# Performance work log

Measured on AMD Instinct MI355X. Metric: run time of the kernel, lower is better.

## Reference

```python
import jax, jax.numpy as jnp
import numpy as np

L, D, H, DFF, V, N, B, C = 4, 512, 8, 2048, 32000, 512, 16, 3
DH = D // H
EPS = 1e-6


def _sinusoid_pe(n, d):
    pos = np.arange(n)[:, None].astype(np.float32)
    div = np.exp(np.arange(0, d, 2).astype(np.float32) * (-np.log(10000.0) / d))
    pe = np.zeros((n, d), np.float32)
    pe[:, 0::2] = np.sin(pos * div)
    pe[:, 1::2] = np.cos(pos * div)
    return jnp.asarray(pe)


def _ln(x, g, b):
    m = x.mean(-1, keepdims=True)
    v = ((x - m) ** 2).mean(-1, keepdims=True)
    return (x - m) * jax.lax.rsqrt(v + EPS) * g + b


def setup_inputs() -> dict:
    key = jax.random.key(0)
    ks = jax.random.split(key, 12)
    rn = lambda k, s: jax.random.normal(k, s, jnp.float32) * 0.02
    return {
        "src": jax.random.randint(ks[0], (N, B, 1), 0, V, jnp.int32),
        "lengths": jnp.full((B,), N, jnp.int32),
        "emb_table": rn(ks[1], (V, D)),
        "ln1_g": jnp.ones((L, D)), "ln1_b": jnp.zeros((L, D)),
        "Wq": rn(ks[2], (L, D, D)), "bq": jnp.zeros((L, D)),
        "Wk": rn(ks[3], (L, D, D)), "bk": jnp.zeros((L, D)),
        "Wv": rn(ks[4], (L, D, D)), "bv": jnp.zeros((L, D)),
        "Wo": rn(ks[5], (L, D, D)), "bo": jnp.zeros((L, D)),
        "ln2_g": jnp.ones((L, D)), "ln2_b": jnp.zeros((L, D)),
        "W1": rn(ks[6], (L, D, DFF)), "b1": jnp.zeros((L, DFF)),
        "W2": rn(ks[7], (L, DFF, D)), "b2": jnp.zeros((L, D)),
        "lnf_g": jnp.ones((D,)), "lnf_b": jnp.zeros((D,)),
        "inf_W": rn(ks[8], (2 * D, C)),
    }


def reference(src, lengths, emb_table, ln1_g, ln1_b, Wq, bq, Wk, bk, Wv, bv,
              Wo, bo, ln2_g, ln2_b, W1, b1, W2, b2, lnf_g, lnf_b, inf_W):
    # embeddings: lookup * sqrt(d) + sinusoidal PE (onmt Embeddings)
    emb = emb_table[src[:, :, 0]] * jnp.sqrt(jnp.float32(D))  # [N,B,D]
    x = (emb + _sinusoid_pe(N, D)[:, None, :]).transpose(1, 0, 2)  # [B,N,D]
    key_pad = jnp.arange(N)[None, :] >= lengths[:, None]  # [B,N] True = pad
    for l in range(L):
        h = _ln(x, ln1_g[l], ln1_b[l])
        q = (h @ Wq[l] + bq[l]).reshape(B, N, H, DH).transpose(0, 2, 1, 3)
        k = (h @ Wk[l] + bk[l]).reshape(B, N, H, DH).transpose(0, 2, 1, 3)
        v = (h @ Wv[l] + bv[l]).reshape(B, N, H, DH).transpose(0, 2, 1, 3)
        scores = jnp.einsum('bhqd,bhkd->bhqk', q, k) / jnp.sqrt(jnp.float32(DH))
        scores = jnp.where(key_pad[:, None, None, :], -1e9, scores)
        attn = jax.nn.softmax(scores, -1)
        ctx = jnp.einsum('bhqk,bhkd->bhqd', attn, v).transpose(0, 2, 1, 3).reshape(B, N, D)
        x = x + ctx @ Wo[l] + bo[l]
        h2 = _ln(x, ln2_g[l], ln2_b[l])
        x = x + jax.nn.relu(h2 @ W1[l] + b1[l]) @ W2[l] + b2[l]
    x = _ln(x, lnf_g, lnf_b)  # [B,N,D]
    attn_res = x.transpose(1, 0, 2)  # [N,B,D]
    # pairwise scorer: Linear(concat(x_i, x_j)) == x_i @ W[:D] + x_j @ W[D:]
    la = x @ inf_W[:D]   # [B,N,C]
    lb = x @ inf_W[D:]   # [B,N,C]
    logits = la[:, :, None, :] + lb[:, None, :, :]  # [B,N,N,C]
    inf_result = jax.nn.log_softmax(logits, -1).reshape(B, N * N, C)
    inf_result = jnp.swapaxes(inf_result, 0, 1)  # [N*N,B,C]
    return (attn_res, inf_result)
```

## Files before the change

kernel.cpp:

```cpp
#include <hip/hip_runtime.h>

constexpr int L = 4, D = 512, H = 8, DFF = 2048, NSEQ = 512, B = 16, C = 3;
constexpr int DH = D / H;
constexpr int M = B * NSEQ;
constexpr int BND = B * NSEQ * D;

typedef short bf16x8 __attribute__((ext_vector_type(8)));
typedef float f32x4 __attribute__((ext_vector_type(4)));

__device__ __forceinline__ float blo(unsigned u) { return __uint_as_float(u << 16); }
__device__ __forceinline__ float bhi(unsigned u) { return __uint_as_float(u & 0xffff0000u); }
__device__ __forceinline__ unsigned short f2b(float f) {
    unsigned u = __float_as_uint(f);
    u += 0x7fffu + ((u >> 16) & 1u);
    return (unsigned short)(u >> 16);
}
__device__ __forceinline__ void gload_lds16(const void* g, void* l) {
    __builtin_amdgcn_global_load_lds(
        (const __attribute__((address_space(1))) void*)g,
        (__attribute__((address_space(3))) void*)l, 16, 0, 0);
}

__device__ __forceinline__ float block_sum256(float v, float* r4) {
#pragma unroll
    for (int o = 32; o > 0; o >>= 1) v += __shfl_xor(v, o, 64);
    if ((threadIdx.x & 63) == 0) r4[threadIdx.x >> 6] = v;
    __syncthreads();
    return r4[0] + r4[1] + r4[2] + r4[3];
}

__global__ __launch_bounds__(256) void conv_t_kernel(
    const float* __restrict__ in, unsigned short* __restrict__ out, int K, int N)
{
    __shared__ float t[32][33];
    int n0 = blockIdx.x * 32, k0 = blockIdx.y * 32;
    const float* ip = in + (size_t)blockIdx.z * K * N;
    unsigned short* op = out + (size_t)blockIdx.z * K * N;
    int tx = threadIdx.x & 31, ty = threadIdx.x >> 5;
#pragma unroll
    for (int i = 0; i < 4; i++)
        t[ty + i * 8][tx] = ip[(size_t)(k0 + ty + i * 8) * N + n0 + tx];
    __syncthreads();
#pragma unroll
    for (int i = 0; i < 4; i++)
        op[(size_t)(n0 + ty + i * 8) * K + k0 + tx] = f2b(t[tx][ty + i * 8]);
}

__global__ __launch_bounds__(256) void embed_pe_kernel(
    const int* __restrict__ src, const float* __restrict__ emb,
    float* __restrict__ x)
{
    int idx = blockIdx.x * 256 + threadIdx.x;
    int d = idx & (D - 1);
    int t = idx >> 9;
    int n = t & (NSEQ - 1);
    int b = t >> 9;
    int tok = src[n * B + b];
    float e = emb[(size_t)tok * D + d] * 22.627416997969522f;
    float div = expf((float)(d & ~1) * -0.01798894603797866f);
    float ang = (float)n * div;
    float pe = (d & 1) ? cosf(ang) : sinf(ang);
    x[idx] = e + pe;
}

template<int BF16OUT>
__global__ __launch_bounds__(256) void ln_kernel(
    const float* __restrict__ in, const float* __restrict__ g,
    const float* __restrict__ bt, void* __restrict__ outv)
{
    __shared__ float ra[4], rb[4];
    int row = blockIdx.x, tid = threadIdx.x;
    const float* p = in + (size_t)row * D;
    float v0 = p[tid], v1 = p[tid + 256];
    float mean = block_sum256(v0 + v1, ra) * (1.0f / D);
    float d0 = v0 - mean, d1 = v1 - mean;
    float var = block_sum256(d0 * d0 + d1 * d1, rb) * (1.0f / D);
    float rstd = rsqrtf(var + 1e-6f);
    float o0 = d0 * rstd * g[tid] + bt[tid];
    float o1 = d1 * rstd * g[tid + 256] + bt[tid + 256];
    if (BF16OUT) {
        unsigned short* o = (unsigned short*)outv + (size_t)row * D;
        o[tid] = f2b(o0); o[tid + 256] = f2b(o1);
    } else {
        float* o = (float*)outv + (size_t)row * D;
        o[tid] = o0; o[tid + 256] = o1;
    }
}

template<int ADD, int RELU, int BF16OUT, int VTRANS>
__global__ __launch_bounds__(256) void mfma_gemm(
    const unsigned short* __restrict__ A,
    const unsigned short* __restrict__ Wt,
    const float* __restrict__ bias,
    void* __restrict__ outv, int Kdim, int Ndim)
{
    __shared__ __align__(16) unsigned short As[128 * 32];
    __shared__ __align__(16) unsigned short Bs[128 * 32];
    int tid = threadIdx.x;
    int wave = tid >> 6, lane = tid & 63;
    int lr = lane & 15, lc = lane >> 4;
    int m0 = blockIdx.y * 128, n0 = blockIdx.x * 128;
    int wm = (wave >> 1) * 64, wn = (wave & 1) * 64;
    int srow = tid >> 2;
    int scol = (tid & 3) << 3;

    const unsigned short* Ab = A + ((size_t)m0 + srow) * Kdim + scol;
    const unsigned short* Bb = Wt + ((size_t)n0 + srow) * Kdim + scol;
    unsigned short* AsW = As + wave * 512;
    unsigned short* BsW = Bs + wave * 512;

    f32x4 acc[4][4] = {};

    for (int kb = 0; kb < Kdim; kb += 32) {
        gload_lds16(Ab + kb, AsW);
        gload_lds16(Ab + kb + (size_t)64 * Kdim, AsW + 2048);
        gload_lds16(Bb + kb, BsW);
        gload_lds16(Bb + kb + (size_t)64 * Kdim, BsW + 2048);
        __syncthreads();

        bf16x8 aF[4], bF[4];
#pragma unroll
        for (int i = 0; i < 4; i++) {
            aF[i] = *reinterpret_cast<const bf16x8*>(&As[(wm + i * 16 + lr) * 32 + lc * 8]);
            bF[i] = *reinterpret_cast<const bf16x8*>(&Bs[(wn + i * 16 + lr) * 32 + lc * 8]);
        }
#pragma unroll
        for (int i = 0; i < 4; i++)
#pragma unroll
            for (int j = 0; j < 4; j++)
                acc[i][j] = __builtin_amdgcn_mfma_f32_16x16x32_bf16(aF[i], bF[j], acc[i][j], 0, 0, 0);
        __syncthreads();
    }

#pragma unroll
    for (int i = 0; i < 4; i++) {
        int grow = m0 + wm + i * 16 + lc * 4;
#pragma unroll
        for (int j = 0; j < 4; j++) {
            int gcol = n0 + wn + j * 16 + lr;
            float bv = bias[gcol];
#pragma unroll
            for (int r = 0; r < 4; r++) {
                float v = acc[i][j][r] + bv;
                if (RELU) v = fmaxf(v, 0.0f);
                if (VTRANS) {
                    int rowg = grow + r;
                    size_t off = ((size_t)((rowg >> 9) << 9) + gcol) * NSEQ + (rowg & (NSEQ - 1));
                    ((unsigned short*)outv)[off] = f2b(v);
                } else {
                    size_t off = (size_t)(grow + r) * Ndim + gcol;
                    if (BF16OUT)      ((unsigned short*)outv)[off] = f2b(v);
                    else if (ADD)     ((float*)outv)[off] += v;
                    else              ((float*)outv)[off] = v;
                }
            }
        }
    }
}

__global__ __launch_bounds__(256, 3) void attn_mfma_kernel(
    const unsigned short* __restrict__ qg, const unsigned short* __restrict__ kg,
    const unsigned short* __restrict__ vtg, const int* __restrict__ lengths,
    unsigned short* __restrict__ ctx)
{
    __shared__ __align__(16) unsigned short Ks[64 * 64];
    __shared__ __align__(16) unsigned short Vt[64 * 64];
    __shared__ __align__(16) unsigned short Ps[64 * 64];

    int tid = threadIdx.x;
    int wave = tid >> 6, lane = tid & 63;
    int lr = lane & 15, lc = lane >> 4;
    int qt = blockIdx.x, hh = blockIdx.y, b = blockIdx.z;
    int len = lengths[b];

    const unsigned short* qbase  = qg  + ((size_t)(b * NSEQ + qt * 64)) * D + hh * DH;
    const unsigned short* kbase  = kg  + ((size_t)(b * NSEQ)) * D + hh * DH;
    const unsigned short* vtbase = vtg + ((size_t)(b * D + hh * DH)) * NSEQ;

    auto SW = [](int row, int colbyte) { return row * 128 + (colbyte ^ ((row & 7) << 4)); };

#pragma unroll
    for (int it = 0; it < 2; it++) {
        int c = it * 256 + tid;
        int row = c >> 3, d0 = (c & 7) << 3;
        uint4 t = *reinterpret_cast<const uint4*>(qbase + (size_t)row * D + d0);
        *reinterpret_cast<uint4*>((char*)Ps + SW(row, d0 * 2)) = t;
    }
    __syncthreads();
    bf16x8 aQ[2];
#pragma unroll
    for (int s = 0; s < 2; s++)
        aQ[s] = *reinterpret_cast<const bf16x8*>((char*)Ps + SW(wave * 16 + lr, s * 64 + lc * 16));

    f32x4 o[4] = {};
    float mrow[4], lrow[4];
#pragma unroll
    for (int r = 0; r < 4; r++) { mrow[r] = -INFINITY; lrow[r] = 0.0f; }

    for (int kt = 0; kt < 8; kt++) {
#pragma unroll
        for (int it = 0; it < 2; it++) {
            int c = it * 256 + tid;
            int row = c >> 3, d0 = (c & 7) << 3;
            uint4 t = *reinterpret_cast<const uint4*>(kbase + (size_t)(kt * 64 + row) * D + d0);
            *reinterpret_cast<uint4*>((char*)Ks + SW(row, d0 * 2)) = t;
            uint4 tv = *reinterpret_cast<const uint4*>(vtbase + (size_t)row * NSEQ + kt * 64 + d0);
            *reinterpret_cast<uint4*>((char*)Vt + SW(row, d0 * 2)) = tv;
        }
        __syncthreads();

        f32x4 sacc[4] = {};
#pragma unroll
        for (int kf = 0; kf < 4; kf++) {
#pragma unroll
            for (int s = 0; s < 2; s++) {
                bf16x8 bK = *reinterpret_cast<const bf16x8*>((char*)Ks + SW(kf * 16 + lr, s * 64 + lc * 16));
                sacc[kf] = __builtin_amdgcn_mfma_f32_16x16x32_bf16(aQ[s], bK, sacc[kf], 0, 0, 0);
            }
        }

        float p[4][4], tm[4];
#pragma unroll
        for (int r = 0; r < 4; r++) tm[r] = -INFINITY;
#pragma unroll
        for (int kf = 0; kf < 4; kf++) {
            int col = kt * 64 + kf * 16 + lr;
            bool ok = col < len;
#pragma unroll
            for (int r = 0; r < 4; r++) {
                float sv = ok ? sacc[kf][r] * 0.125f : -1e9f;
                p[kf][r] = sv;
                tm[r] = fmaxf(tm[r], sv);
            }
        }
#pragma unroll
        for (int r = 0; r < 4; r++) {
#pragma unroll
            for (int msk = 1; msk < 16; msk <<= 1)
                tm[r] = fmaxf(tm[r], __shfl_xor(tm[r], msk, 64));
        }
        float alpha[4], ps[4];
#pragma unroll
        for (int r = 0; r < 4; r++) {
            float nm = fmaxf(mrow[r], tm[r]);
            alpha[r] = __expf(mrow[r] - nm);
            mrow[r] = nm;
            ps[r] = 0.0f;
        }
#pragma unroll
        for (int kf = 0; kf < 4; kf++)
#pragma unroll
            for (int r = 0; r < 4; r++) {
                float e = __expf(p[kf][r] - mrow[r]);
                p[kf][r] = e;
                ps[r] += e;
            }
#pragma unroll
        for (int r = 0; r < 4; r++) {
#pragma unroll
            for (int msk = 1; msk < 16; msk <<= 1)
                ps[r] += __shfl_xor(ps[r], msk, 64);
            lrow[r] = lrow[r] * alpha[r] + ps[r];
        }

#pragma unroll
        for (int kf = 0; kf < 4; kf++)
#pragma unroll
            for (int r = 0; r < 4; r++)
                *reinterpret_cast<unsigned short*>(
                    (char*)Ps + SW(wave * 16 + lc * 4 + r, (kf * 16 + lr) * 2)) = f2b(p[kf][r]);

#pragma unroll
        for (int df = 0; df < 4; df++)
#pragma unroll
            for (int r = 0; r < 4; r++)
                o[df][r] *= alpha[r];

#pragma unroll
        for (int s = 0; s < 2; s++) {
            bf16x8 pa = *reinterpret_cast<const bf16x8*>((char*)Ps + SW(wave * 16 + lr, s * 64 + lc * 16));
#pragma unroll
            for (int df = 0; df < 4; df++) {
                bf16x8 vb = *reinterpret_cast<const bf16x8*>((char*)Vt + SW(df * 16 + lr, s * 64 + lc * 16));
                o[df] = __builtin_amdgcn_mfma_f32_16x16x32_bf16(pa, vb, o[df], 0, 0, 0);
            }
        }
        __syncthreads();
    }

    unsigned short* obase = ctx + ((size_t)(b * NSEQ + qt * 64 + wave * 16)) * D + hh * DH;
#pragma unroll
    for (int r = 0; r < 4; r++) {
        float inv = 1.0f / lrow[r];
        int q = lc * 4 + r;
#pragma unroll
        for (int df = 0; df < 4; df++)
            obase[(size_t)q * D + df * 16 + lr] = f2b(o[df][r] * inv);
    }
}

__global__ __launch_bounds__(256) void store_attnres(
    const float* __restrict__ hf, float* __restrict__ out)
{
    int idx = blockIdx.x * 256 + threadIdx.x;
    int d  = idx & (D - 1);
    int nb = idx >> 9;
    int b  = nb & (B - 1);
    int n  = nb >> 4;
    out[idx] = hf[((size_t)(b * NSEQ + n)) * D + d];
}

__global__ __launch_bounds__(256) void lalb_kernel(
    const float* __restrict__ hf, const float* __restrict__ infW,
    float* __restrict__ la, float* __restrict__ lb)
{
    __shared__ float r24[24];
    int t = blockIdx.x, tid = threadIdx.x;
    const float* p = hf + (size_t)t * D;
    float x0 = p[tid], x1 = p[tid + 256];
    float s[6];
#pragma unroll
    for (int c = 0; c < 3; c++) {
        s[c]     = x0 * infW[(size_t)tid * C + c]         + x1 * infW[(size_t)(tid + 256) * C + c];
        s[3 + c] = x0 * infW[(size_t)(tid + 512) * C + c] + x1 * infW[(size_t)(tid + 768) * C + c];
    }
#pragma unroll
    for (int c = 0; c < 6; c++)
#pragma unroll
        for (int o = 32; o > 0; o >>= 1) s[c] += __shfl_xor(s[c], o, 64);
    if ((tid & 63) == 0) {
#pragma unroll
        for (int c = 0; c < 6; c++) r24[c * 4 + (tid >> 6)] = s[c];
    }
    __syncthreads();
    if (tid < 6) {
        float v = r24[tid * 4] + r24[tid * 4 + 1] + r24[tid * 4 + 2] + r24[tid * 4 + 3];
        if (tid < 3) la[(size_t)t * C + tid] = v;
        else         lb[(size_t)t * C + tid - 3] = v;
    }
}

__global__ __launch_bounds__(256) void logits_kernel(
    const float* __restrict__ la, const float* __restrict__ lb,
    float* __restrict__ out)
{
    int idx = blockIdx.x * 256 + threadIdx.x;
    int b  = idx & (B - 1);
    int ij = idx >> 4;
    int j  = ij & (NSEQ - 1);
    int i  = ij >> 9;
    const float* pa = la + ((size_t)(b * NSEQ + i)) * C;
    const float* pb = lb + ((size_t)(b * NSEQ + j)) * C;
    float l0 = pa[0] + pb[0];
    float l1 = pa[1] + pb[1];
    float l2 = pa[2] + pb[2];
    float m = fmaxf(l0, fmaxf(l1, l2));
    float lse = m + logf(__expf(l0 - m) + __expf(l1 - m) + __expf(l2 - m));
    out[(size_t)idx * 3 + 0] = l0 - lse;
    out[(size_t)idx * 3 + 1] = l1 - lse;
    out[(size_t)idx * 3 + 2] = l2 - lse;
}

extern "C" void kernel_launch(void* const* d_in, const int* in_sizes, int n_in,
                              void* d_out, int out_size, void* d_ws, size_t ws_size,
                              hipStream_t stream)
{
    const int*   src     = (const int*)  d_in[0];
    const int*   lengths = (const int*)  d_in[1];
    const float* emb     = (const float*)d_in[2];
    const float* ln1_g   = (const float*)d_in[3];
    const float* ln1_b   = (const float*)d_in[4];
    const float* Wq      = (const float*)d_in[5];
    const float* bq      = (const float*)d_in[6];
    const float* Wk      = (const float*)d_in[7];
    const float* bk      = (const float*)d_in[8];
    const float* Wv      = (const float*)d_in[9];
    const float* bv      = (const float*)d_in[10];
    const float* Wo      = (const float*)d_in[11];
    const float* bo      = (const float*)d_in[12];
    const float* ln2_g   = (const float*)d_in[13];
    const float* ln2_b   = (const float*)d_in[14];
    const float* W1      = (const float*)d_in[15];
    const float* b1      = (const float*)d_in[16];
    const float* W2      = (const float*)d_in[17];
    const float* b2      = (const float*)d_in[18];
    const float* lnf_g   = (const float*)d_in[19];
    const float* lnf_b   = (const float*)d_in[20];
    const float* infW    = (const float*)d_in[21];

    char* wsb = (char*)d_ws;
    float*          x   = (float*)wsb;
    unsigned short* h   = (unsigned short*)(wsb + (size_t)BND * 4);
    unsigned short* wts = (unsigned short*)(wsb + (size_t)BND * 4 + (size_t)BND * 2);
    char*           big = wsb + (size_t)BND * 4 + (size_t)BND * 2 + 25165824;

    unsigned short* qbm = (unsigned short*)big;
    unsigned short* kbm = qbm + (size_t)M * D;
    unsigned short* vtm = kbm + (size_t)M * D;
    unsigned short* ffh = (unsigned short*)big;
    float*          hf  = (float*)big;
    float*          la  = hf + BND;
    float*          lb  = la + (size_t)M * C;

    unsigned short* WQt = wts;
    unsigned short* WKt = WQt + (size_t)L * D * D;
    unsigned short* WVt = WKt + (size_t)L * D * D;
    unsigned short* WOt = WVt + (size_t)L * D * D;
    unsigned short* W1t = WOt + (size_t)L * D * D;
    unsigned short* W2t = W1t + (size_t)L * D * DFF;

    dim3 blk(256);

    conv_t_kernel<<<dim3(D / 32, D / 32, L), blk, 0, stream>>>(Wq, WQt, D, D);
    conv_t_kernel<<<dim3(D / 32, D / 32, L), blk, 0, stream>>>(Wk, WKt, D, D);
    conv_t_kernel<<<dim3(D / 32, D / 32, L), blk, 0, stream>>>(Wv, WVt, D, D);
    conv_t_kernel<<<dim3(D / 32, D / 32, L), blk, 0, stream>>>(Wo, WOt, D, D);
    conv_t_kernel<<<dim3(DFF / 32, D / 32, L), blk, 0, stream>>>(W1, W1t, D, DFF);
    conv_t_kernel<<<dim3(D / 32, DFF / 32, L), blk, 0, stream>>>(W2, W2t, DFF, D);

    embed_pe_kernel<<<BND / 256, blk, 0, stream>>>(src, emb, x);

    dim3 gdd(D / 128, M / 128);
    dim3 gdf(DFF / 128, M / 128);
    dim3 gattn(NSEQ / 64, H, B);

    for (int l = 0; l < L; l++) {
        size_t bd = (size_t)l * D, wdd = (size_t)l * D * D;
        size_t wdf = (size_t)l * D * DFF, bf1 = (size_t)l * DFF;
        ln_kernel<1><<<M, blk, 0, stream>>>(x, ln1_g + bd, ln1_b + bd, h);
        mfma_gemm<0, 0, 1, 0><<<gdd, blk, 0, stream>>>(h, WQt + wdd, bq + bd, qbm, D, D);
        mfma_gemm<0, 0, 1, 0><<<gdd, blk, 0, stream>>>(h, WKt + wdd, bk + bd, kbm, D, D);
        mfma_gemm<0, 0, 1, 1><<<gdd, blk, 0, stream>>>(h, WVt + wdd, bv + bd, vtm, D, D);
        attn_mfma_kernel<<<gattn, blk, 0, stream>>>(qbm, kbm, vtm, lengths, h);
        mfma_gemm<1, 0, 0, 0><<<gdd, blk, 0, stream>>>(h, WOt + wdd, bo + bd, x, D, D);
        ln_kernel<1><<<M, blk, 0, stream>>>(x, ln2_g + bd, ln2_b + bd, h);
        mfma_gemm<0, 1, 1, 0><<<gdf, blk, 0, stream>>>(h, W1t + wdf, b1 + bf1, ffh, D, DFF);
        mfma_gemm<1, 0, 0, 0><<<gdd, blk, 0, stream>>>(ffh, W2t + wdf, b2 + bd, x, DFF, D);
    }

    ln_kernel<0><<<M, blk, 0, stream>>>(x, lnf_g, lnf_b, hf);
    store_attnres<<<(NSEQ * B * D) / 256, blk, 0, stream>>>(hf, (float*)d_out);
    lalb_kernel<<<M, blk, 0, stream>>>(hf, infW, la, lb);
    logits_kernel<<<(NSEQ * NSEQ * B) / 256, blk, 0, stream>>>(
        la, lb, (float*)d_out + (size_t)NSEQ * B * D);
}
```

Before: 1.134 ms.

## Fuse QKV projections into one GEMM and split-K the residual GEMMs

Stores the Q, K and V weights in one interleaved [3D x D] transposed buffer, so a single GEMM launch with a per-column epilogue writes Q, K and the transposed V. The Wo and W2 residual GEMMs are split along K into 2 and 4 parts, with the partial results accumulated into x using float atomicAdd. This cuts launch count and adds blocks to the under-filled 512-wide GEMMs (256 tiles before). The cost is atomic traffic on x and a summation order that is no longer deterministic.

```diff
diff --git a/kernel.cpp b/kernel.cpp
--- a/kernel.cpp
+++ b/kernel.cpp
@@ -30,12 +30,13 @@
 }
 
 __global__ __launch_bounds__(256) void conv_t_kernel(
-    const float* __restrict__ in, unsigned short* __restrict__ out, int K, int N)
+    const float* __restrict__ in, unsigned short* __restrict__ out,
+    int K, int N, int lstride)
 {
     __shared__ float t[32][33];
     int n0 = blockIdx.x * 32, k0 = blockIdx.y * 32;
     const float* ip = in + (size_t)blockIdx.z * K * N;
-    unsigned short* op = out + (size_t)blockIdx.z * K * N;
+    unsigned short* op = out + (size_t)blockIdx.z * lstride;
     int tx = threadIdx.x & 31, ty = threadIdx.x >> 5;
 #pragma unroll
     for (int i = 0; i < 4; i++)
@@ -87,12 +88,14 @@
     }
 }
 
-template<int ADD, int RELU, int BF16OUT, int VTRANS>
+template<int EPI, int SPLITK>
 __global__ __launch_bounds__(256) void mfma_gemm(
     const unsigned short* __restrict__ A,
     const unsigned short* __restrict__ Wt,
-    const float* __restrict__ bias,
-    void* __restrict__ outv, int Kdim, int Ndim)
+    const float* __restrict__ biasQ, const float* __restrict__ biasK,
+    const float* __restrict__ biasV,
+    void* __restrict__ out0, void* __restrict__ out1, void* __restrict__ out2,
+    int Kdim, int Ndim)
 {
     __shared__ __align__(16) unsigned short As[128 * 32];
     __shared__ __align__(16) unsigned short Bs[128 * 32];
@@ -100,6 +103,7 @@
     int wave = tid >> 6, lane = tid & 63;
     int lr = lane & 15, lc = lane >> 4;
     int m0 = blockIdx.y * 128, n0 = blockIdx.x * 128;
+    int kz = blockIdx.z;
     int wm = (wave >> 1) * 64, wn = (wave & 1) * 64;
     int srow = tid >> 2;
     int scol = (tid & 3) << 3;
@@ -109,9 +113,12 @@
     unsigned short* AsW = As + wave * 512;
     unsigned short* BsW = Bs + wave * 512;
 
+    int kpart = Kdim / SPLITK;
+    int kbeg = kz * kpart, kend = kbeg + kpart;
+
     f32x4 acc[4][4] = {};
 
-    for (int kb = 0; kb < Kdim; kb += 32) {
+    for (int kb = kbeg; kb < kend; kb += 32) {
         gload_lds16(Ab + kb, AsW);
         gload_lds16(Ab + kb + (size_t)64 * Kdim, AsW + 2048);
         gload_lds16(Bb + kb, BsW);
@@ -138,20 +145,32 @@
 #pragma unroll
         for (int j = 0; j < 4; j++) {
             int gcol = n0 + wn + j * 16 + lr;
-            float bv = bias[gcol];
+            float bv;
+            if (EPI == 3)
+                bv = (gcol < D) ? biasQ[gcol]
+                   : (gcol < 2 * D) ? biasK[gcol - D] : biasV[gcol - 2 * D];
+            else
+                bv = (EPI == 0 && kz != 0) ? 0.0f : biasQ[gcol];
 #pragma unroll
             for (int r = 0; r < 4; r++) {
                 float v = acc[i][j][r] + bv;
-                if (RELU) v = fmaxf(v, 0.0f);
-                if (VTRANS) {
-                    int rowg = grow + r;
-                    size_t off = ((size_t)((rowg >> 9) << 9) + gcol) * NSEQ + (rowg & (NSEQ - 1));
-                    ((unsigned short*)outv)[off] = f2b(v);
+                if (EPI == 2) v = fmaxf(v, 0.0f);
+                int tok = grow + r;
+                if (EPI == 0) {
+                    float* op = (float*)out0 + (size_t)tok * Ndim + gcol;
+                    if (SPLITK > 1) atomicAdd(op, v); else *op += v;
+                } else if (EPI == 3) {
+                    if (gcol < D)
+                        ((unsigned short*)out0)[(size_t)tok * D + gcol] = f2b(v);
+                    else if (gcol < 2 * D)
+                        ((unsigned short*)out1)[(size_t)tok * D + gcol - D] = f2b(v);
+                    else {
+                        int dcol = gcol - 2 * D;
+                        ((unsigned short*)out2)[
+                            (((size_t)(tok >> 9) << 9) + dcol) * NSEQ + (tok & (NSEQ - 1))] = f2b(v);
+                    }
                 } else {
-                    size_t off = (size_t)(grow + r) * Ndim + gcol;
-                    if (BF16OUT)      ((unsigned short*)outv)[off] = f2b(v);
-                    else if (ADD)     ((float*)outv)[off] += v;
-                    else              ((float*)outv)[off] = v;
+                    ((unsigned short*)out0)[(size_t)tok * Ndim + gcol] = f2b(v);
                 }
             }
         }
@@ -402,40 +421,43 @@
     float*          la  = hf + BND;
     float*          lb  = la + (size_t)M * C;
 
-    unsigned short* WQt = wts;
-    unsigned short* WKt = WQt + (size_t)L * D * D;
-    unsigned short* WVt = WKt + (size_t)L * D * D;
-    unsigned short* WOt = WVt + (size_t)L * D * D;
-    unsigned short* W1t = WOt + (size_t)L * D * D;
-    unsigned short* W2t = W1t + (size_t)L * D * DFF;
+    unsigned short* QKVt = wts;
+    unsigned short* WOt  = QKVt + (size_t)L * 3 * D * D;
+    unsigned short* W1t  = WOt + (size_t)L * D * D;
+    unsigned short* W2t  = W1t + (size_t)L * D * DFF;
 
     dim3 blk(256);
 
-    conv_t_kernel<<<dim3(D / 32, D / 32, L), blk, 0, stream>>>(Wq, WQt, D, D);
-    conv_t_kernel<<<dim3(D / 32, D / 32, L), blk, 0, stream>>>(Wk, WKt, D, D);
-    conv_t_kernel<<<dim3(D / 32, D / 32, L), blk, 0, stream>>>(Wv, WVt, D, D);
-    conv_t_kernel<<<dim3(D / 32, D / 32, L), blk, 0, stream>>>(Wo, WOt, D, D);
-    conv_t_kernel<<<dim3(DFF / 32, D / 32, L), blk, 0, stream>>>(W1, W1t, D, DFF);
-    conv_t_kernel<<<dim3(D / 32, DFF / 32, L), blk, 0, stream>>>(W2, W2t, DFF, D);
+    conv_t_kernel<<<dim3(D / 32, D / 32, L), blk, 0, stream>>>(Wq, QKVt,             D, D, 3 * D * D);
+    conv_t_kernel<<<dim3(D / 32, D / 32, L), blk, 0, stream>>>(Wk, QKVt + D * D,     D, D, 3 * D * D);
+    conv_t_kernel<<<dim3(D / 32, D / 32, L), blk, 0, stream>>>(Wv, QKVt + 2 * D * D, D, D, 3 * D * D);
+    conv_t_kernel<<<dim3(D / 32, D / 32, L), blk, 0, stream>>>(Wo, WOt, D, D, D * D);
+    conv_t_kernel<<<dim3(DFF / 32, D / 32, L), blk, 0, stream>>>(W1, W1t, D, DFF, D * DFF);
+    conv_t_kernel<<<dim3(D / 32, DFF / 32, L), blk, 0, stream>>>(W2, W2t, DFF, D, DFF * D);
 
     embed_pe_kernel<<<BND / 256, blk, 0, stream>>>(src, emb, x);
 
-    dim3 gdd(D / 128, M / 128);
-    dim3 gdf(DFF / 128, M / 128);
+    dim3 gqkv(3 * D / 128, M / 128);
+    dim3 gwo(D / 128, M / 128, 2);
+    dim3 gw1(DFF / 128, M / 128);
+    dim3 gw2(D / 128, M / 128, 4);
     dim3 gattn(NSEQ / 64, H, B);
 
     for (int l = 0; l < L; l++) {
-        size_t bd = (size_t)l * D, wdd = (size_t)l * D * D;
+        size_t bd = (size_t)l * D;
+        size_t wqkv = (size_t)l * 3 * D * D, wdd = (size_t)l * D * D;
         size_t wdf = (size_t)l * D * DFF, bf1 = (size_t)l * DFF;
         ln_kernel<1><<<M, blk, 0, stream>>>(x, ln1_g + bd, ln1_b + bd, h);
-        mfma_gemm<0, 0, 1, 0><<<gdd, blk, 0, stream>>>(h, WQt + wdd, bq + bd, qbm, D, D);
-        mfma_gemm<0, 0, 1, 0><<<gdd, blk, 0, stream>>>(h, WKt + wdd, bk + bd, kbm, D, D);
-        mfma_gemm<0, 0, 1, 1><<<gdd, blk, 0, stream>>>(h, WVt + wdd, bv + bd, vtm, D, D);
+        mfma_gemm<3, 1><<<gqkv, blk, 0, stream>>>(
+            h, QKVt + wqkv, bq + bd, bk + bd, bv + bd, qbm, kbm, vtm, D, 3 * D);
         attn_mfma_kernel<<<gattn, blk, 0, stream>>>(qbm, kbm, vtm, lengths, h);
-        mfma_gemm<1, 0, 0, 0><<<gdd, blk, 0, stream>>>(h, WOt + wdd, bo + bd, x, D, D);
+        mfma_gemm<0, 2><<<gwo, blk, 0, stream>>>(
+            h, WOt + wdd, bo + bd, nullptr, nullptr, x, nullptr, nullptr, D, D);
         ln_kernel<1><<<M, blk, 0, stream>>>(x, ln2_g + bd, ln2_b + bd, h);
-        mfma_gemm<0, 1, 1, 0><<<gdf, blk, 0, stream>>>(h, W1t + wdf, b1 + bf1, ffh, D, DFF);
-        mfma_gemm<1, 0, 0, 0><<<gdd, blk, 0, stream>>>(ffh, W2t + wdf, b2 + bd, x, DFF, D);
+        mfma_gemm<2, 1><<<gw1, blk, 0, stream>>>(
+            h, W1t + wdf, b1 + bf1, nullptr, nullptr, ffh, nullptr, nullptr, D, DFF);
+        mfma_gemm<0, 4><<<gw2, blk, 0, stream>>>(
+            ffh, W2t + wdf, b2 + bd, nullptr, nullptr, x, nullptr, nullptr, DFF, D);
     }
 
     ln_kernel<0><<<M, blk, 0, stream>>>(x, lnf_g, lnf_b, hf);
```

Result: slower. 1.163 ms (+2.5%).
